# Kernel optimization log

Hardware: AMD Instinct MI355X
Metric: run time of the kernel (lower is better)

The kernel has to match this reference:

```python
import jax, jax.numpy as jnp
import numpy as np

N_NODES, N_EDGES, BATCH = 50000, 100000, 256
H = 64            # dim_hidden_features
D_NODE, D_EDGE, D_RBF = 110, 8, 8
D_SET = 2 * H     # Set2Set input_dim = 128, output_dim = 256
D_HID = 512
D_CAT = 54
MP_STEPS, S2S_ITERS = 4, 3


def setup_inputs() -> dict:
    key = jax.random.key(0)
    ks = iter(jax.random.split(key, 48))

    def nrm(shape, s=0.05):
        return jax.random.normal(next(ks), shape, dtype=jnp.float32) * s

    inp = {}
    inp["node_attribute"] = jax.random.normal(next(ks), (N_NODES, D_NODE), dtype=jnp.float32)
    inp["edge_attribute"] = jax.random.normal(next(ks), (N_EDGES, D_EDGE), dtype=jnp.float32)
    inp["edge_length"] = jax.random.uniform(next(ks), (N_EDGES,), dtype=jnp.float32)
    inp["src"] = jax.random.randint(next(ks), (N_EDGES,), 0, N_NODES, dtype=jnp.int32)
    inp["dst"] = jax.random.randint(next(ks), (N_EDGES,), 0, N_NODES, dtype=jnp.int32)
    inp["node_graph"] = jnp.sort(jax.random.randint(next(ks), (N_NODES,), 0, BATCH, dtype=jnp.int32))
    # atom_feature_projector
    inp["proj_W"] = nrm((D_NODE, H)); inp["proj_b"] = jnp.zeros((H,), jnp.float32)
    # RBF layer: centers ~ U(0,1), beta = 10 (per reset_parameters)
    inp["centers"] = jax.random.uniform(next(ks), (D_RBF,), dtype=jnp.float32)
    inp["beta"] = jnp.full((D_RBF,), 10.0, jnp.float32)
    # NNConv edge function: Linear(16 -> 64*64), plus NNConv bias
    inp["bond_W"] = nrm((D_EDGE + D_RBF, H * H)); inp["bond_b"] = jnp.zeros((H * H,), jnp.float32)
    inp["conv_b"] = jnp.zeros((H,), jnp.float32)
    # GRU (input H, hidden H); PyTorch layout (3H, in)
    inp["gru_Wih"] = nrm((3 * H, H)); inp["gru_Whh"] = nrm((3 * H, H))
    inp["gru_bih"] = jnp.zeros((3 * H,), jnp.float32); inp["gru_bhh"] = jnp.zeros((3 * H,), jnp.float32)
    # Set2Set LSTM: input 2*D_SET=256, hidden D_SET=128, 2 layers; PyTorch layout (4H, in)
    inp["lstm_Wih0"] = nrm((4 * D_SET, 2 * D_SET)); inp["lstm_Whh0"] = nrm((4 * D_SET, D_SET))
    inp["lstm_bih0"] = jnp.zeros((4 * D_SET,), jnp.float32); inp["lstm_bhh0"] = jnp.zeros((4 * D_SET,), jnp.float32)
    inp["lstm_Wih1"] = nrm((4 * D_SET, D_SET)); inp["lstm_Whh1"] = nrm((4 * D_SET, D_SET))
    inp["lstm_bih1"] = jnp.zeros((4 * D_SET,), jnp.float32); inp["lstm_bhh1"] = jnp.zeros((4 * D_SET,), jnp.float32)
    # sparsify: Linear(256 -> 512) + PReLU(init 0.25)
    inp["sp_W"] = nrm((2 * D_SET, D_HID)); inp["sp_b"] = jnp.zeros((D_HID,), jnp.float32)
    inp["prelu_a"] = jnp.array([0.25], jnp.float32)
    # catalyst1 head: hiddens[0] (512->512 ReLU, 512->512 Tanh) then outputs[0] (512->54)
    inp["h0_W1"] = nrm((D_HID, D_HID)); inp["h0_b1"] = jnp.zeros((D_HID,), jnp.float32)
    inp["h0_W2"] = nrm((D_HID, D_HID)); inp["h0_b2"] = jnp.zeros((D_HID,), jnp.float32)
    inp["out_W"] = nrm((D_HID, D_CAT)); inp["out_b"] = jnp.zeros((D_CAT,), jnp.float32)
    return inp


def _lstm_cell(x, h, c, Wih, Whh, bih, bhh):
    # PyTorch LSTM gate order: i, f, g, o
    g = x @ Wih.T + bih + h @ Whh.T + bhh
    i, f, gg, o = jnp.split(g, 4, axis=-1)
    c = jax.nn.sigmoid(f) * c + jax.nn.sigmoid(i) * jnp.tanh(gg)
    h = jax.nn.sigmoid(o) * jnp.tanh(c)
    return h, c


def reference(node_attribute, edge_attribute, edge_length, src, dst, node_graph,
              proj_W, proj_b, centers, beta, bond_W, bond_b, conv_b,
              gru_Wih, gru_Whh, gru_bih, gru_bhh,
              lstm_Wih0, lstm_Whh0, lstm_bih0, lstm_bhh0,
              lstm_Wih1, lstm_Whh1, lstm_bih1, lstm_bhh1,
              sp_W, sp_b, prelu_a, h0_W1, h0_b1, h0_W2, h0_b2, out_W, out_b):
    n_nodes = node_attribute.shape[0]
    # atom feature projection
    x = jax.nn.relu(node_attribute @ proj_W + proj_b)                       # (N, H)
    # edge features = [edge_attribute, RBF(length)]
    rbf = jnp.exp(-beta * (edge_length[:, None] - centers[None, :]) ** 2)   # (E, 8)
    efeat = jnp.concatenate([edge_attribute, rbf], axis=-1)                 # (E, 16)
    # NNConv per-edge weight matrix; edge features are constant over MP steps
    W_e = (efeat @ bond_W + bond_b).reshape(-1, H, H)                       # (E, H, H)

    feat, h = x, x
    for _ in range(MP_STEPS):
        # NNConv: message = h_src @ W_e, sum-aggregated at dst, plus bias
        m = jnp.einsum('ei,eio->eo', feat[src], W_e)                        # (E, H)
        agg = jax.ops.segment_sum(m, dst, num_segments=n_nodes) + conv_b    # (N, H)
        gx = jax.nn.relu(agg)
        # GRU cell (PyTorch gate order r, z, n)
        gi = gx @ gru_Wih.T + gru_bih
        gh = h @ gru_Whh.T + gru_bhh
        i_r, i_z, i_n = jnp.split(gi, 3, axis=-1)
        h_r, h_z, h_n = jnp.split(gh, 3, axis=-1)
        r = jax.nn.sigmoid(i_r + h_r)
        z = jax.nn.sigmoid(i_z + h_z)
        n = jnp.tanh(i_n + r * h_n)
        h = (1.0 - z) * n + z * h
        feat = h
    node_agg = jnp.concatenate([feat, x], axis=-1)                          # (N, 2H)

    # Set2Set pooling over graphs (segment softmax attention, 2-layer LSTM)
    B = BATCH
    h0 = c0 = jnp.zeros((B, D_SET), node_agg.dtype)
    h1 = c1 = jnp.zeros((B, D_SET), node_agg.dtype)
    q_star = jnp.zeros((B, 2 * D_SET), node_agg.dtype)
    for _ in range(S2S_ITERS):
        h0, c0 = _lstm_cell(q_star, h0, c0, lstm_Wih0, lstm_Whh0, lstm_bih0, lstm_bhh0)
        h1, c1 = _lstm_cell(h0, h1, c1, lstm_Wih1, lstm_Whh1, lstm_bih1, lstm_bhh1)
        q = h1                                                              # (B, 128)
        e = jnp.sum(node_agg * q[node_graph], axis=-1)                      # (N,)
        emax = jax.ops.segment_max(e, node_graph, num_segments=B)
        p = jnp.exp(e - emax[node_graph])
        denom = jax.ops.segment_sum(p, node_graph, num_segments=B)
        alpha = p / denom[node_graph]                                       # per-graph softmax
        r_out = jax.ops.segment_sum(node_agg * alpha[:, None], node_graph, num_segments=B)
        q_star = jnp.concatenate([q, r_out], axis=-1)                       # (B, 256)

    # sparsify (Linear + PReLU)
    feats = q_star @ sp_W + sp_b                                            # (B, 512)
    feats = jnp.where(feats >= 0, feats, prelu_a * feats)
    # catalyst1 head
    hid = jnp.tanh(jax.nn.relu(feats @ h0_W1 + h0_b1) @ h0_W2 + h0_b2)
    return jax.nn.softmax(hid @ out_W + out_b, axis=-1)                     # (B, 54)
```

## Files before the change

kernel.cpp:

```cpp
#include <hip/hip_runtime.h>
#include <math.h>

constexpr int N = 50000;
constexpr int E = 100000;
constexpr int B = 256;
constexpr int H = 64;
constexpr int DN = 110;
constexpr int NBLK = (E + 63) / 64;

#define DEV __device__ __forceinline__

typedef __attribute__((ext_vector_type(8))) short short8;
typedef __attribute__((ext_vector_type(4))) float floatx4;

DEV float sigf(float x) { return 1.0f / (1.0f + expf(-x)); }

DEV short f2bf(float f) {
    unsigned u = __float_as_uint(f);
    unsigned r = (u + 0x7fffu + ((u >> 16) & 1u)) >> 16;
    return (short)r;
}
DEV float bf2f(short s) { return __uint_as_float(((unsigned)(unsigned short)s) << 16); }

DEV void cvt8(const float* p, short8& hi, short8& lo) {
// ... 26 lines not shown
    int t = idx >> 6;
    int ntile = t % NT16;
    int kt = t / NT16;
    int quad = lane >> 4, col = lane & 15;
    int o = ntile * 16 + col;
    short hi[8], lo[8];
#pragma unroll
    for (int j = 0; j < 8; ++j) {
        int k = kt * 32 + quad * 8 + j;
        float v = 0.0f;
        if (o < ocap && k < kcap) v = trans ? W[(size_t)o * ld + k] : W[(size_t)k * ld + o];
        short hb = f2bf(v);
        hi[j] = hb;
        lo[j] = f2bf(v - bf2f(hb));
    }
    short* dh = out + (((size_t)(t * 2 + 0) * 64 + lane) * 8);
    short* dl = out + (((size_t)(t * 2 + 1) * 64 + lane) * 8);
#pragma unroll
    for (int j = 0; j < 8; ++j) { dh[j] = hi[j]; dl[j] = lo[j]; }
}

DEV void d_prepW(const float* __restrict__ bond_W, const float* __restrict__ bond_b,
                 short* __restrict__ wf, int idx) {
    int lane = idx & 63;
    int t = idx >> 6;
    int ks = t & 1;
    int nt = (t >> 1) & 3;
    int kk = t >> 3;
    const float* S = (kk < 16) ? (bond_W + kk * 4096) : bond_b;
    int quad = lane >> 4, col = lane & 15;
    short hi[8], lo[8];
#pragma unroll
    for (int j = 0; j < 8; ++j) {
        int i = ks * 32 + quad * 8 + j;
        float v = S[i * 64 + nt * 16 + col];
        short hb = f2bf(v);
        hi[j] = hb;
        lo[j] = f2bf(v - bf2f(hb));
    }
    short* dh = wf + (((size_t)(t * 2 + 0) * 64 + lane) * 8);
    short* dl = wf + (((size_t)(t * 2 + 1) * 64 + lane) * 8);
#pragma unroll
    for (int j = 0; j < 8; ++j) { dh[j] = hi[j]; dl[j] = lo[j]; }
}

__launch_bounds__(256)
__global__ void k_prep0(const float* lWih0, const float* lWhh0, const float* lWih1, const float* lWhh1,
                        float* lW0P, float* lU0P, float* lW1P, float* lU1P,
                        const float* bond_W, const float* bond_b, short* wf,
                        const float* gru_Wih, const float* gru_Whh, short* fgI, short* fgH,
                        const float* proj_W, short* fproj,
                        const float* ea, const float* el, const float* centers,
                        const float* beta, const int* epos, float* ef_t,
                        const int* ng, int* gs, int* ge,
                        float* zreg) {
    int idx = blockIdx.x * 256 + threadIdx.x;
    if (idx < 65536) { d_packpair(lWih0, lW0P, 256, idx); return; }
    idx -= 65536;
    if (idx < 32768) { d_packpair(lWhh0, lU0P, 128, idx); return; }
    idx -= 32768;
    if (idx < 32768) { d_packpair(lWih1, lW1P, 128, idx); return; }
    idx -= 32768;
    if (idx < 32768) { d_packpair(lWhh1, lU1P, 128, idx); return; }
    idx -= 32768;
    if (idx < 8704) { d_prepW(bond_W, bond_b, wf, idx); return; }
    idx -= 8704;
    if (idx < 1536) { d_prepB(gru_Wih, fgI, 12, 64, 1, 192, 64, idx); return; }
    idx -= 1536;
    if (idx < 1536) { d_prepB(gru_Whh, fgH, 12, 64, 1, 192, 64, idx); return; }
    idx -= 1536;
    if (idx < 1024) { d_prepB(proj_W, fproj, 4, 64, 0, 64, DN, idx); return; }
    idx -= 1024;
    if (idx < E) {
        int e = idx;
        int pos = epos[e];
        float L = el[e];
#pragma unroll
        for (int j = 0; j < 8; ++j) ef_t[(size_t)j * E + pos] = ea[e * 8 + j];
#pragma unroll
        for (int j = 0; j < 8; ++j) {
            float d = L - centers[j];
            ef_t[(size_t)(8 + j) * E + pos] = expf(-beta[j] * d * d);
        }
        ef_t[(size_t)16 * E + pos] = 1.0f;
        return;
    }
    idx -= E;
    if (idx < N) {
        int n = idx;
        int g = ng[n];
        int gp = (n == 0) ? -1 : ng[n - 1];
        if (g != gp) {
            gs[g] = n;
            if (n > 0) ge[gp] = n;
            for (int q = gp + 1; q < g; ++q) { gs[q] = 0; ge[q] = 0; }
        }
        if (n == N - 1) {
            ge[g] = N;
            for (int q = g + 1; q < B; ++q) { gs[q] = 0; ge[q] = 0; }
        }
        return;
    }
    idx -= N;
    if (idx < 196608) { zreg[idx] = 0.0f; return; }
}
constexpr int PREP0_TOTAL = 65536 + 3 * 32768 + 8704 + 2 * 1536 + 1024 + E + N + 196608;

__launch_bounds__(256)
__global__ void k_prephead(const float* sp_W, short* fsp, const float* h0_W1, short* fw1,
                           const float* h0_W2, short* fw2, const float* out_W, short* fow) {
    int idx = blockIdx.x * 256 + threadIdx.x;
    if (idx < 16384) { d_prepB(sp_W, fsp, 32, 512, 0, 512, 256, idx); return; }
    idx -= 16384;
    if (idx < 32768) { d_prepB(h0_W1, fw1, 32, 512, 0, 512, 512, idx); return; }
    idx -= 32768;
    if (idx < 32768) { d_prepB(h0_W2, fw2, 32, 512, 0, 512, 512, idx); return; }
    idx -= 32768;
    if (idx < 4096) { d_prepB(out_W, fow, 4, 54, 0, 54, 512, idx); return; }
}
constexpr int PREPH_TOTAL = 16384 + 2 * 32768 + 4096;

__global__ void k_deg(const int* __restrict__ dst, int* __restrict__ deg) {
    int e = blockIdx.x * 256 + threadIdx.x;
    if (e < E) atomicAdd(&deg[dst[e]], 1);
}
__global__ void k_scan1(const int* __restrict__ deg, int* __restrict__ bsum) {
    __shared__ int s[256];
    int b = blockIdx.x, tid = threadIdx.x;
    int idx = b * 256 + tid;
    s[tid] = (idx < N) ? deg[idx] : 0;
    __syncthreads();
    for (int st = 128; st > 0; st >>= 1) {
        if (tid < st) s[tid] += s[tid + st];
        __syncthreads();
    }
    if (tid == 0) bsum[b] = s[0];
}
__global__ void k_scan2p(int* __restrict__ bsum, int nb) {
    __shared__ int s[256];
    int tid = threadIdx.x;
    int v = (tid < nb) ? bsum[tid] : 0;
    s[tid] = v;
    __syncthreads();
    for (int off = 1; off < 256; off <<= 1) {
        int t = (tid >= off) ? s[tid - off] : 0;
        __syncthreads();
        s[tid] += t;
        __syncthreads();
    }
    if (tid < nb) bsum[tid] = s[tid] - v;
}
__global__ void k_scan3(const int* __restrict__ deg, const int* __restrict__ bsum,
                        int* __restrict__ cursor, int* __restrict__ roff) {
    __shared__ int s[256];
    int b = blockIdx.x, tid = threadIdx.x;
    int idx = b * 256 + tid;
    int v = (idx < N) ? deg[idx] : 0;
    s[tid] = v;
    __syncthreads();
    for (int off = 1; off < 256; off <<= 1) {
        int t = (tid >= off) ? s[tid - off] : 0;
        __syncthreads();
        s[tid] += t;
        __syncthreads();
    }
    if (idx < N) {
        int start = bsum[b] + s[tid] - v;
        cursor[idx] = start;
        roff[idx] = start;
    }
    if (idx == 0) roff[N] = E;
}
__global__ void k_scat(const int* __restrict__ src, const int* __restrict__ dst,
// ... 13 lines not shown
                        const float* __restrict__ b, float* __restrict__ x,
                        short* __restrict__ hs) {
    __shared__ float as[16 * 132];
    int tid = threadIdx.x, lane = tid & 63, nt = tid >> 6;
    int quad = lane >> 4, col = lane & 15;
    int s0 = blockIdx.x * 16;
    for (int i = tid; i < 16 * DN; i += 256) {
        int r = i / DN, c = i % DN;
        as[r * 132 + c] = na[(size_t)s0 * DN + i];
    }
    for (int i = tid; i < 16 * 22; i += 256) {
        int r = i / 22, c = DN + i % 22;
        as[r * 132 + c] = 0.0f;
    }
    __syncthreads();
    const short8* F = (const short8*)fp;
    floatx4 T = {0.0f, 0.0f, 0.0f, 0.0f};
#pragma unroll
    for (int kt = 0; kt < 4; ++kt) {
        const float* ap = as + col * 132 + kt * 32 + quad * 8;
        short8 ah, al;
#pragma unroll
        for (int j = 0; j < 8; ++j) {
            float v = ap[j];
            short hb = f2bf(v);
            ah[j] = hb;
            al[j] = f2bf(v - bf2f(hb));
        }
        int t = kt * 4 + nt;
        short8 bh = F[(t * 2 + 0) * 64 + lane];
        short8 bl = F[(t * 2 + 1) * 64 + lane];
        T = __builtin_amdgcn_mfma_f32_16x16x32_bf16(ah, bh, T, 0, 0, 0);
        T = __builtin_amdgcn_mfma_f32_16x16x32_bf16(al, bh, T, 0, 0, 0);
        T = __builtin_amdgcn_mfma_f32_16x16x32_bf16(ah, bl, T, 0, 0, 0);
    }
    int o = nt * 16 + col;
    float bo = b[o];
#pragma unroll
    for (int r = 0; r < 4; ++r) {
        int n = s0 + quad * 4 + r;
        float v = fmaxf(T[r] + bo, 0.0f);
        x[(size_t)n * 64 + o] = v;
        short hb = f2bf(v);
        hs[(size_t)n * 128 + o] = hb;
        hs[(size_t)n * 128 + 64 + o] = f2bf(v - bf2f(hb));
    }
}

__launch_bounds__(256)
__global__ void k_msgagg(const short* __restrict__ hs, const float* __restrict__ ef_t,
                         const short* __restrict__ wf, const int* __restrict__ srcp,
                         const int* __restrict__ dstp,
                         float* __restrict__ agg, float* __restrict__ bpart) {
    __shared__ int dsh[64];
    __shared__ int shprev;
    __shared__ float Csh[64][68];

    int tid = threadIdx.x;
    int e0 = blockIdx.x * 64;
    int lane = tid & 63;
    int nt = tid >> 6;
    int quad = lane >> 4, col = lane & 15;

    if (tid < 64) {
        int eg = e0 + tid;
        dsh[tid] = (eg < E) ? dstp[eg] : N;
    }
    if (tid == 0) shprev = (e0 == 0) ? -1 : dstp[e0 - 1];

    short8 Ah[4][2], Al[4][2];
#pragma unroll
    for (int mt = 0; mt < 4; ++mt) {
        int eg = e0 + mt * 16 + col;
        int s = (eg < E) ? srcp[eg] : 0;
        const short* hp = hs + (size_t)s * 128 + quad * 8;
#pragma unroll
        for (int ks = 0; ks < 2; ++ks) {
            Ah[mt][ks] = *(const short8*)(hp + ks * 32);
            Al[mt][ks] = *(const short8*)(hp + 64 + ks * 32);
        }
    }

    const short8* Wf = (const short8*)wf;
    const float* efb = ef_t + e0 + quad * 4;
    float C[4][4] = {};

#define LOADB(d0, d1, d2, d3, KK)                      \
    {                                                  \
        int tb_ = ((KK) * 4 + nt) * 2;                 \
        d0 = Wf[((tb_ + 0) * 2 + 0) * 64 + lane];      \
        d1 = Wf[((tb_ + 1) * 2 + 0) * 64 + lane];      \
        d2 = Wf[((tb_ + 0) * 2 + 1) * 64 + lane];      \
        d3 = Wf[((tb_ + 1) * 2 + 1) * 64 + lane];      \
    }

    short8 c0, c1, c2, c3, n0_, n1_, n2_, n3_, q0, q1, q2, q3;
    LOADB(c0, c1, c2, c3, 0);
    LOADB(n0_, n1_, n2_, n3_, 1);
    LOADB(q0, q1, q2, q3, 2);

#pragma unroll 1
    for (int kk = 0; kk < 17; ++kk) {
        int kn = kk + 3;
        if (kn > 16) kn = 16;
        short8 p0, p1, p2, p3;
        LOADB(p0, p1, p2, p3, kn);

        float4 ef0 = *(const float4*)(efb + (size_t)kk * E + 0);
        float4 ef1 = *(const float4*)(efb + (size_t)kk * E + 16);
        float4 ef2 = *(const float4*)(efb + (size_t)kk * E + 32);
        float4 ef3 = *(const float4*)(efb + (size_t)kk * E + 48);
        float4 efv[4] = {ef0, ef1, ef2, ef3};

#pragma unroll
        for (int mt = 0; mt < 4; ++mt) {
            floatx4 T = {0.0f, 0.0f, 0.0f, 0.0f};
            T = __builtin_amdgcn_mfma_f32_16x16x32_bf16(Ah[mt][0], c0, T, 0, 0, 0);
            T = __builtin_amdgcn_mfma_f32_16x16x32_bf16(Ah[mt][1], c1, T, 0, 0, 0);
            T = __builtin_amdgcn_mfma_f32_16x16x32_bf16(Al[mt][0], c0, T, 0, 0, 0);
            T = __builtin_amdgcn_mfma_f32_16x16x32_bf16(Al[mt][1], c1, T, 0, 0, 0);
            T = __builtin_amdgcn_mfma_f32_16x16x32_bf16(Ah[mt][0], c2, T, 0, 0, 0);
            T = __builtin_amdgcn_mfma_f32_16x16x32_bf16(Ah[mt][1], c3, T, 0, 0, 0);
            C[mt][0] += efv[mt].x * T[0];
            C[mt][1] += efv[mt].y * T[1];
            C[mt][2] += efv[mt].z * T[2];
            C[mt][3] += efv[mt].w * T[3];
        }
        c0 = n0_; c1 = n1_; c2 = n2_; c3 = n3_;
        n0_ = q0; n1_ = q1; n2_ = q2; n3_ = q3;
        q0 = p0; q1 = p1; q2 = p2; q3 = p3;
    }
#undef LOADB

#pragma unroll
    for (int mt = 0; mt < 4; ++mt)
#pragma unroll
        for (int r = 0; r < 4; ++r)
            Csh[mt * 16 + quad * 4 + r][nt * 16 + col] = C[mt][r];
    __syncthreads();

    if (tid < 64) {
        int c = tid;
        int prevd = shprev;
        int firstd = dsh[0];
        for (int q = prevd + 1; q < firstd; ++q) agg[(size_t)q * 64 + c] = 0.0f;
        int cur = firstd;
        float acc = 0.0f;
        bool owned = (e0 == 0) || (firstd != prevd);
        bool done = false;
        for (int r = 0; r < 64; ++r) {
            int d = dsh[r];
            if (d != cur) {
                if (owned) agg[(size_t)cur * 64 + c] = acc;
                else bpart[(size_t)blockIdx.x * 64 + c] = acc;
                int dc = (d < N) ? d : N;
                for (int q = cur + 1; q < dc; ++q) agg[(size_t)q * 64 + c] = 0.0f;
                cur = d;
                acc = 0.0f;
                owned = true;
                if (cur >= N) { done = true; break; }
            }
            acc += Csh[r][c];
        }
        if (!done) {
            if (owned) agg[(size_t)cur * 64 + c] = acc;
            else bpart[(size_t)blockIdx.x * 64 + c] = acc;
        }
    }
}

__launch_bounds__(256)
__global__ void k_gru4(const float* agg, const float* __restrict__ bpart,
                       const int* __restrict__ roff, const float* __restrict__ conv_b,
                       short* __restrict__ hs,
                       const short* __restrict__ fI, const short* __restrict__ fH,
                       const float* __restrict__ bih, const float* __restrict__ bhh,
                       float* hf) {
    __shared__ float aggS[32 * 65];
    __shared__ short hsS[32 * 132];
// ... 100 lines not shown
                aH[mt][g] = __builtin_amdgcn_mfma_f32_16x16x32_bf16(Hh[mt][ks], bHl[g], aH[mt][g], 0, 0, 0);
            }
        }
    }

    int o = nt * 16 + col;
    float br = bih[o], bz = bih[64 + o], bn = bih[128 + o];
    float cr = bhh[o], cz = bhh[64 + o], cn = bhh[128 + o];
#pragma unroll
    for (int mt = 0; mt < 2; ++mt) {
#pragma unroll
        for (int r = 0; r < 4; ++r) {
            int row = mt * 16 + quad * 4 + r;
            float rg = sigf(aI[mt][0][r] + br + aH[mt][0][r] + cr);
            float z  = sigf(aI[mt][1][r] + bz + aH[mt][1][r] + cz);
            float ng = tanhf(aI[mt][2][r] + bn + rg * (aH[mt][2][r] + cn));
            float hold = bf2f(hsS[row * 132 + o]) + bf2f(hsS[row * 132 + 64 + o]);
            aggS[row * 65 + o] = (1.0f - z) * ng + z * hold;
        }
    }
    __syncthreads();

#pragma unroll
    for (int it = 0; it < 2; ++it) {
        int i = tid * 8 + it * 2048;
        int r = i >> 7, c = i & 127;
        int node = n0 + r;
        if (node < N) {
            bool hiP = (c < 64);
            int f0 = hiP ? c : (c - 64);
            short8 v;
#pragma unroll
            for (int j = 0; j < 8; ++j) {
                float hv = aggS[r * 65 + f0 + j];
                short hb = f2bf(hv);
                v[j] = hiP ? hb : f2bf(hv - bf2f(hb));
            }
            *(short8*)(hs + (size_t)node * 128 + c) = v;
        }
    }
    if (hf) {
#pragma unroll
        for (int it = 0; it < 2; ++it) {
            int i = tid * 4 + it * 1024;
            int r = i >> 6, c = i & 63;
            int node = n0 + r;
            if (node < N)
                *(float4*)(hf + (size_t)node * 64 + c) = *(const float4*)&aggS[r * 65 + c];
        }
    }
}

__launch_bounds__(256)
__global__ void k_s2s(float* __restrict__ h0, float* __restrict__ c0,
                      float* __restrict__ h1, float* __restrict__ c1,
                      float* __restrict__ q_star,
                      const float* __restrict__ W0P, const float* __restrict__ U0P,
                      const float* __restrict__ b0i, const float* __restrict__ b0h,
                      const float* __restrict__ W1P, const float* __restrict__ U1P,
                      const float* __restrict__ b1i, const float* __restrict__ b1h,
                      const float* __restrict__ hf, const float* __restrict__ x,
                      const int* __restrict__ gs, const int* __restrict__ ge) {
    __shared__ float xb[256], hb[128], gb[512], h0n[128], qv[128];
    __shared__ float mrg[4][2][64];
    __shared__ float ml[4][2];
    int g = blockIdx.x, tid = threadIdx.x;
    xb[tid] = q_star[g * 256 + tid];
    if (tid < 128) hb[tid] = h0[g * 128 + tid];
    __syncthreads();
    float g0 = b0i[tid] + b0h[tid];
    float g1 = b0i[tid + 256] + b0h[tid + 256];
    for (int i = 0; i < 256; ++i) {
        float xx = xb[i];
        float2 w = *(const float2*)(W0P + 2 * (i * 256 + tid));
        g0 += xx * w.x;
        g1 += xx * w.y;
    }
    for (int i = 0; i < 128; ++i) {
        float hh = hb[i];
        float2 w = *(const float2*)(U0P + 2 * (i * 256 + tid));
        g0 += hh * w.x;
        g1 += hh * w.y;
    }
    gb[tid] = g0; gb[tid + 256] = g1;
    __syncthreads();
    if (tid < 128) {
        float ii = gb[tid], ff = gb[128 + tid], gg = gb[256 + tid], oo = gb[384 + tid];
        float c = sigf(ff) * c0[g * 128 + tid] + sigf(ii) * tanhf(gg);
        float hn = sigf(oo) * tanhf(c);
        c0[g * 128 + tid] = c; h0[g * 128 + tid] = hn; h0n[tid] = hn;
        hb[tid] = h1[g * 128 + tid];
    }
    __syncthreads();
    float ga = b1i[tid] + b1h[tid];
    float gbv = b1i[tid + 256] + b1h[tid + 256];
    for (int i = 0; i < 128; ++i) {
        float xx = h0n[i], hh = hb[i];
        float2 w1 = *(const float2*)(W1P + 2 * (i * 256 + tid));
        float2 u1 = *(const float2*)(U1P + 2 * (i * 256 + tid));
        ga  += xx * w1.x + hh * u1.x;
        gbv += xx * w1.y + hh * u1.y;
    }
    gb[tid] = ga; gb[tid + 256] = gbv;
    __syncthreads();
    if (tid < 128) {
        float ii = gb[tid], ff = gb[128 + tid], gg = gb[256 + tid], oo = gb[384 + tid];
        float c = sigf(ff) * c1[g * 128 + tid] + sigf(ii) * tanhf(gg);
        float hn = sigf(oo) * tanhf(c);
        c1[g * 128 + tid] = c; h1[g * 128 + tid] = hn;
        q_star[g * 256 + tid] = hn;
        qv[tid] = hn;
    }
    __syncthreads();
    int s0v = gs[g], s1v = ge[g];
    int lane = tid & 63, grp = tid >> 6;
    float qh = qv[lane], qx = qv[64 + lane];
    float mM = -INFINITY, lL = 0.0f, nh = 0.0f, nx = 0.0f;
    for (int n = s0v + grp; n < s1v; n += 16) {
        float hv[4], xv[4], e[4];
#pragma unroll
        for (int j = 0; j < 4; ++j) {
            int nj = n + 4 * j;
            int nc = (nj < s1v) ? nj : n;
            hv[j] = hf[(size_t)nc * 64 + lane];
            xv[j] = x[(size_t)nc * 64 + lane];
            e[j] = hv[j] * qh + xv[j] * qx;
        }
#pragma unroll
        for (int off = 32; off; off >>= 1) {
#pragma unroll
            for (int j = 0; j < 4; ++j) e[j] += __shfl_xor(e[j], off, 64);
        }
#pragma unroll
        for (int j = 0; j < 4; ++j)
            if (n + 4 * j >= s1v) e[j] = -INFINITY;
        float mb = fmaxf(fmaxf(e[0], e[1]), fmaxf(e[2], e[3]));
        float mn = fmaxf(mM, mb);
        float sc = expf(mM - mn);
        float w0 = expf(e[0] - mn), w1 = expf(e[1] - mn);
        float w2 = expf(e[2] - mn), w3 = expf(e[3] - mn);
        lL = lL * sc + ((w0 + w1) + (w2 + w3));
        nh = nh * sc + ((w0 * hv[0] + w1 * hv[1]) + (w2 * hv[2] + w3 * hv[3]));
        nx = nx * sc + ((w0 * xv[0] + w1 * xv[1]) + (w2 * xv[2] + w3 * xv[3]));
        mM = mn;
    }
    mrg[grp][0][lane] = nh;
    mrg[grp][1][lane] = nx;
    if (lane == 0) { ml[grp][0] = mM; ml[grp][1] = lL; }
    __syncthreads();
    if (tid < 128) {
        int half = tid >> 6, dl = tid & 63;
        float M = -INFINITY;
#pragma unroll
        for (int i = 0; i < 4; ++i) M = fmaxf(M, ml[i][0]);
        float L = 0.0f, NUM = 0.0f;
#pragma unroll
        for (int i = 0; i < 4; ++i) {
            float sc = expf(ml[i][0] - M);
            L += ml[i][1] * sc;
            NUM += mrg[i][half][dl] * sc;
        }
        q_star[g * 256 + 128 + tid] = (s1v > s0v) ? NUM / L : 0.0f;
    }
}

template<int MODE>
__launch_bounds__(256)
__global__ void k_hgemm(const float* __restrict__ A, const short* __restrict__ Bf,
                        const float* __restrict__ bias, const float* __restrict__ pa,
                        float* __restrict__ Cout, int K, int NT16) {
    int tid = threadIdx.x, lane = tid & 63, nt = tid >> 6;
    int quad = lane >> 4, col = lane & 15;
    int s0 = blockIdx.x * 16;
    int ntile = blockIdx.y * 4 + nt;
    int NoutTot = NT16 * 16;
    const short8* F = (const short8*)Bf;
    floatx4 T = {0.0f, 0.0f, 0.0f, 0.0f};
    const float* ap = A + (size_t)(s0 + col) * K + quad * 8;
    int KT = K >> 5;
#pragma unroll 4
    for (int kt = 0; kt < KT; ++kt) {
        short8 ah, al;
        cvt8(ap + kt * 32, ah, al);
        int t = kt * NT16 + ntile;
        short8 bh = F[(t * 2 + 0) * 64 + lane];
        short8 bl = F[(t * 2 + 1) * 64 + lane];
        T = __builtin_amdgcn_mfma_f32_16x16x32_bf16(ah, bh, T, 0, 0, 0);
        T = __builtin_amdgcn_mfma_f32_16x16x32_bf16(al, bh, T, 0, 0, 0);
        T = __builtin_amdgcn_mfma_f32_16x16x32_bf16(ah, bl, T, 0, 0, 0);
    }
    int o = ntile * 16 + col;
    float b = bias[o];
    float a = (MODE == 0) ? pa[0] : 0.0f;
#pragma unroll
    for (int r = 0; r < 4; ++r) {
        float v = T[r] + b;
        if (MODE == 0) v = (v >= 0.0f) ? v : a * v;
        if (MODE == 1) v = fmaxf(v, 0.0f);
        if (MODE == 2) v = tanhf(v);
        Cout[(size_t)(s0 + quad * 4 + r) * NoutTot + o] = v;
    }
}

__launch_bounds__(256)
__global__ void k_hout(const float* __restrict__ A, const short* __restrict__ Bf,
                       const float* __restrict__ ob, float* __restrict__ out) {
    __shared__ float sm[16][64];
    __shared__ float smax[16], sinv[16];
    int tid = threadIdx.x, lane = tid & 63, nt = tid >> 6;
    int quad = lane >> 4, col = lane & 15;
    int s0 = blockIdx.x * 16;
    const short8* F = (const short8*)Bf;
    floatx4 T = {0.0f, 0.0f, 0.0f, 0.0f};
    const float* ap = A + (size_t)(s0 + col) * 512 + quad * 8;
#pragma unroll 4
    for (int kt = 0; kt < 16; ++kt) {
        short8 ah, al;
        cvt8(ap + kt * 32, ah, al);
        int t = kt * 4 + nt;
        short8 bh = F[(t * 2 + 0) * 64 + lane];
        short8 bl = F[(t * 2 + 1) * 64 + lane];
        T = __builtin_amdgcn_mfma_f32_16x16x32_bf16(ah, bh, T, 0, 0, 0);
        T = __builtin_amdgcn_mfma_f32_16x16x32_bf16(al, bh, T, 0, 0, 0);
        T = __builtin_amdgcn_mfma_f32_16x16x32_bf16(ah, bl, T, 0, 0, 0);
    }
    int o = nt * 16 + col;
    float b = (o < 54) ? ob[o] : 0.0f;
#pragma unroll
    for (int r = 0; r < 4; ++r)
        sm[quad * 4 + r][o] = (o < 54) ? (T[r] + b) : -1e30f;
    __syncthreads();
    if (tid < 16) {
        float m = -INFINITY;
        for (int j = 0; j < 54; ++j) m = fmaxf(m, sm[tid][j]);
        float s = 0.0f;
        for (int j = 0; j < 54; ++j) s += expf(sm[tid][j] - m);
        smax[tid] = m;
        sinv[tid] = 1.0f / s;
    }
    __syncthreads();
    for (int idx = tid; idx < 16 * 54; idx += 256) {
        int srow = idx / 54, oo = idx % 54;
        out[(size_t)(s0 + srow) * 54 + oo] = expf(sm[srow][oo] - smax[srow]) * sinv[srow];
    }
}

extern "C" void kernel_launch(void* const* d_in, const int* in_sizes, int n_in,
                              void* d_out, int out_size, void* d_ws, size_t ws_size,
                              hipStream_t stream) {
    const float* node_attr = (const float*)d_in[0];
    const float* edge_attr = (const float*)d_in[1];
    const float* edge_len  = (const float*)d_in[2];
    const int*   src       = (const int*)d_in[3];
    const int*   dst       = (const int*)d_in[4];
    const int*   node_grph = (const int*)d_in[5];
    const float* proj_W    = (const float*)d_in[6];
    const float* proj_b    = (const float*)d_in[7];
    const float* centers   = (const float*)d_in[8];
    const float* beta      = (const float*)d_in[9];
    const float* bond_W    = (const float*)d_in[10];
    const float* bond_b    = (const float*)d_in[11];
    const float* conv_b    = (const float*)d_in[12];
    const float* gru_Wih   = (const float*)d_in[13];
    const float* gru_Whh   = (const float*)d_in[14];
    const float* gru_bih   = (const float*)d_in[15];
    const float* gru_bhh   = (const float*)d_in[16];
    const float* lWih0     = (const float*)d_in[17];
    const float* lWhh0     = (const float*)d_in[18];
    const float* lbih0     = (const float*)d_in[19];
    const float* lbhh0     = (const float*)d_in[20];
    const float* lWih1     = (const float*)d_in[21];
    const float* lWhh1     = (const float*)d_in[22];
    const float* lbih1     = (const float*)d_in[23];
    const float* lbhh1     = (const float*)d_in[24];
    const float* sp_W      = (const float*)d_in[25];
    const float* sp_b      = (const float*)d_in[26];
    const float* prelu_a   = (const float*)d_in[27];
    const float* h0_W1     = (const float*)d_in[28];
    const float* h0_b1     = (const float*)d_in[29];
    const float* h0_W2     = (const float*)d_in[30];
    const float* h0_b2     = (const float*)d_in[31];
    const float* out_W     = (const float*)d_in[32];
    const float* out_b     = (const float*)d_in[33];
    float* out = (float*)d_out;

    float* ws = (float*)d_ws;
    size_t off = 0;
    float* x      = ws + off; off += (size_t)N * 64;
    float* hsf    = ws + off; off += (size_t)N * 64;
    float* ef_t   = ws + off; off += (size_t)E * 17;
    float* agg    = ws + off; off += (size_t)N * 64;
    float* wfrag  = ws + off; off += 17 * 16 * 64 * 8 / 2;
    float* fgI    = ws + off; off += 2 * 64 * 192 / 2;
    float* fgH    = ws + off; off += 2 * 64 * 192 / 2;
    float* fproj  = ws + off; off += 16 * 1024 / 2;
    float* lW0P   = ws + off; off += 256 * 512;
    float* lU0P   = ws + off; off += 128 * 512;
    float* lW1P   = ws + off; off += 128 * 512;
    float* lU1P   = ws + off; off += 128 * 512;
    float* h0     = ws + off; off += B * 128;
    float* c0     = ws + off; off += B * 128;
    float* h1     = ws + off; off += B * 128;
    float* c1     = ws + off; off += B * 128;
    float* q_star = ws + off; off += B * 256;
    float* bpart  = ws + off; off += (size_t)NBLK * 64;
    int* gs       = (int*)(ws + off); off += B;
    int* ge       = (int*)(ws + off); off += B;
    int* deg      = (int*)(ws + off); off += N;
    int* cursor   = (int*)(ws + off); off += N;
    int* roff     = (int*)(ws + off); off += N + 1;
    int* bsum     = (int*)(ws + off); off += 256;
    int* srcp     = (int*)(ws + off); off += E;
    int* epos     = (int*)(ws + off); off += E;
    int* dstp     = (int*)(ws + off); off += E;

    short* hs = (short*)hsf;

    short* fsp = (short*)ef_t;
    short* fw1 = (short*)(ef_t + 131072);
    short* fw2 = (short*)(ef_t + 131072 + 262144);
    short* fow = (short*)(ef_t + 131072 + 2 * 262144);
    float* hb1 = ef_t + 131072 + 2 * 262144 + 32768;
    float* hb2 = hb1 + 131072;

    constexpr int NB = (N + 255) / 256;

    k_izero<<<NB, 256, 0, stream>>>(deg, N);
    k_deg<<<(E + 255) / 256, 256, 0, stream>>>(dst, deg);
    k_scan1<<<NB, 256, 0, stream>>>(deg, bsum);
    k_scan2p<<<1, 256, 0, stream>>>(bsum, NB);
    k_scan3<<<NB, 256, 0, stream>>>(deg, bsum, cursor, roff);
    k_scat<<<(E + 255) / 256, 256, 0, stream>>>(src, dst, cursor, srcp, epos, dstp);

    k_prep0<<<(PREP0_TOTAL + 255) / 256, 256, 0, stream>>>(
        lWih0, lWhh0, lWih1, lWhh1, lW0P, lU0P, lW1P, lU1P,
        bond_W, bond_b, (short*)wfrag, gru_Wih, gru_Whh, (short*)fgI, (short*)fgH,
        proj_W, (short*)fproj,
        edge_attr, edge_len, centers, beta, epos, ef_t,
        node_grph, gs, ge, h0);

    k_projm<<<N / 16, 256, 0, stream>>>(node_attr, (const short*)fproj, proj_b, x, hs);

    for (int step = 0; step < 4; ++step) {
        k_msgagg<<<NBLK, 256, 0, stream>>>(hs, ef_t, (const short*)wfrag, srcp, dstp,
                                           agg, bpart);
        k_gru4<<<(N + 31) / 32, 256, 0, stream>>>(agg, bpart, roff, conv_b, hs,
                                                  (const short*)fgI, (const short*)fgH,
                                                  gru_bih, gru_bhh,
                                                  (step == 3) ? agg : nullptr);
    }

    k_prephead<<<(PREPH_TOTAL + 255) / 256, 256, 0, stream>>>(
        sp_W, fsp, h0_W1, fw1, h0_W2, fw2, out_W, fow);

    for (int it = 0; it < 3; ++it) {
        k_s2s<<<B, 256, 0, stream>>>(h0, c0, h1, c1, q_star,
                                     lW0P, lU0P, lbih0, lbhh0,
                                     lW1P, lU1P, lbih1, lbhh1,
                                     agg, x, gs, ge);
    }

    k_hgemm<0><<<dim3(16, 8), 256, 0, stream>>>(q_star, fsp, sp_b, prelu_a, hb1, 256, 32);
    k_hgemm<1><<<dim3(16, 8), 256, 0, stream>>>(hb1, fw1, h0_b1, nullptr, hb2, 512, 32);
    k_hgemm<2><<<dim3(16, 8), 256, 0, stream>>>(hb2, fw2, h0_b2, nullptr, hb1, 512, 32);
    k_hout<<<16, 256, 0, stream>>>(hb1, fow, out_b, out);
}
```

Before: 696.6 us.

## Fuse Set2Set iterations and head GEMMs into single kernels, stage edge features in LDS

The three Set2Set launches are merged into one kernel that keeps the LSTM state in shared memory and skips the matmuls against zero state on the first iteration. The head weight prep is folded into the tail of that kernel. The four head GEMM launches become one kernel that keeps its activations in LDS. In the message kernel, edge features and source indices are staged into shared memory before the MFMA loop instead of being loaded from global memory inside it. The aim is to cut launch count, global round-trips of intermediates and the zeroing pass, at the cost of more LDS use and an extra barrier in the message kernel.

```diff
diff --git a/kernel.cpp b/kernel.cpp
--- a/kernel.cpp
+++ b/kernel.cpp
@@ -102,8 +102,7 @@
                         const float* proj_W, short* fproj,
                         const float* ea, const float* el, const float* centers,
                         const float* beta, const int* epos, float* ef_t,
-                        const int* ng, int* gs, int* ge,
-                        float* zreg) {
+                        const int* ng, int* gs, int* ge) {
     int idx = blockIdx.x * 256 + threadIdx.x;
     if (idx < 65536) { d_packpair(lWih0, lW0P, 256, idx); return; }
     idx -= 65536;
@@ -151,24 +150,8 @@
         }
         return;
     }
-    idx -= N;
-    if (idx < 196608) { zreg[idx] = 0.0f; return; }
-}
-constexpr int PREP0_TOTAL = 65536 + 3 * 32768 + 8704 + 2 * 1536 + 1024 + E + N + 196608;
-
-__launch_bounds__(256)
-__global__ void k_prephead(const float* sp_W, short* fsp, const float* h0_W1, short* fw1,
-                           const float* h0_W2, short* fw2, const float* out_W, short* fow) {
-    int idx = blockIdx.x * 256 + threadIdx.x;
-    if (idx < 16384) { d_prepB(sp_W, fsp, 32, 512, 0, 512, 256, idx); return; }
-    idx -= 16384;
-    if (idx < 32768) { d_prepB(h0_W1, fw1, 32, 512, 0, 512, 512, idx); return; }
-    idx -= 32768;
-    if (idx < 32768) { d_prepB(h0_W2, fw2, 32, 512, 0, 512, 512, idx); return; }
-    idx -= 32768;
-    if (idx < 4096) { d_prepB(out_W, fow, 4, 54, 0, 54, 512, idx); return; }
-}
-constexpr int PREPH_TOTAL = 16384 + 2 * 32768 + 4096;
+}
+constexpr int PREP0_TOTAL = 65536 + 3 * 32768 + 8704 + 2 * 1536 + 1024 + E + N;
 
 __global__ void k_deg(const int* __restrict__ dst, int* __restrict__ deg) {
     int e = blockIdx.x * 256 + threadIdx.x;
@@ -288,6 +271,8 @@
                          const short* __restrict__ wf, const int* __restrict__ srcp,
                          const int* __restrict__ dstp,
                          float* __restrict__ agg, float* __restrict__ bpart) {
+    __shared__ float efs[17 * 64];
+    __shared__ int srcs[64];
     __shared__ int dsh[64];
     __shared__ int shprev;
     __shared__ float Csh[64][68];
@@ -300,15 +285,21 @@
 
     if (tid < 64) {
         int eg = e0 + tid;
+        srcs[tid] = (eg < E) ? srcp[eg] : 0;
         dsh[tid] = (eg < E) ? dstp[eg] : N;
     }
     if (tid == 0) shprev = (e0 == 0) ? -1 : dstp[e0 - 1];
+    for (int i = tid; i < 17 * 64; i += 256) {
+        int kk = i >> 6, e = i & 63;
+        int eg = e0 + e;
+        efs[i] = (eg < E) ? ef_t[(size_t)kk * E + eg] : 0.0f;
+    }
+    __syncthreads();
 
     short8 Ah[4][2], Al[4][2];
 #pragma unroll
     for (int mt = 0; mt < 4; ++mt) {
-        int eg = e0 + mt * 16 + col;
-        int s = (eg < E) ? srcp[eg] : 0;
+        int s = srcs[mt * 16 + col];
         const short* hp = hs + (size_t)s * 128 + quad * 8;
 #pragma unroll
         for (int ks = 0; ks < 2; ++ks) {
@@ -318,7 +309,6 @@
     }
 
     const short8* Wf = (const short8*)wf;
-    const float* efb = ef_t + e0 + quad * 4;
     float C[4][4] = {};
 
 #define LOADB(d0, d1, d2, d3, KK)                      \
@@ -341,12 +331,6 @@
         if (kn > 16) kn = 16;
         short8 p0, p1, p2, p3;
         LOADB(p0, p1, p2, p3, kn);
-
-        float4 ef0 = *(const float4*)(efb + (size_t)kk * E + 0);
-        float4 ef1 = *(const float4*)(efb + (size_t)kk * E + 16);
-        float4 ef2 = *(const float4*)(efb + (size_t)kk * E + 32);
-        float4 ef3 = *(const float4*)(efb + (size_t)kk * E + 48);
-        float4 efv[4] = {ef0, ef1, ef2, ef3};
 
 #pragma unroll
         for (int mt = 0; mt < 4; ++mt) {
@@ -357,10 +341,11 @@
             T = __builtin_amdgcn_mfma_f32_16x16x32_bf16(Al[mt][1], c1, T, 0, 0, 0);
             T = __builtin_amdgcn_mfma_f32_16x16x32_bf16(Ah[mt][0], c2, T, 0, 0, 0);
             T = __builtin_amdgcn_mfma_f32_16x16x32_bf16(Ah[mt][1], c3, T, 0, 0, 0);
-            C[mt][0] += efv[mt].x * T[0];
-            C[mt][1] += efv[mt].y * T[1];
-            C[mt][2] += efv[mt].z * T[2];
-            C[mt][3] += efv[mt].w * T[3];
+            float4 ef = *(const float4*)&efs[kk * 64 + mt * 16 + quad * 4];
+            C[mt][0] += ef.x * T[0];
+            C[mt][1] += ef.y * T[1];
+            C[mt][2] += ef.z * T[2];
+            C[mt][3] += ef.w * T[3];
         }
         c0 = n0_; c1 = n1_; c2 = n2_; c3 = n3_;
         n0_ = q0; n1_ = q1; n2_ = q2; n3_ = q3;
@@ -567,183 +552,265 @@
 }
 
 __launch_bounds__(256)
-__global__ void k_s2s(float* __restrict__ h0, float* __restrict__ c0,
-                      float* __restrict__ h1, float* __restrict__ c1,
-                      float* __restrict__ q_star,
-                      const float* __restrict__ W0P, const float* __restrict__ U0P,
-                      const float* __restrict__ b0i, const float* __restrict__ b0h,
-                      const float* __restrict__ W1P, const float* __restrict__ U1P,
-                      const float* __restrict__ b1i, const float* __restrict__ b1h,
-                      const float* __restrict__ hf, const float* __restrict__ x,
-                      const int* __restrict__ gs, const int* __restrict__ ge) {
-    __shared__ float xb[256], hb[128], gb[512], h0n[128], qv[128];
+__global__ void k_s2s3(float* __restrict__ q_star,
+                       const float* __restrict__ W0P, const float* __restrict__ U0P,
+                       const float* __restrict__ b0i, const float* __restrict__ b0h,
+                       const float* __restrict__ W1P, const float* __restrict__ U1P,
+                       const float* __restrict__ b1i, const float* __restrict__ b1h,
+                       const float* __restrict__ hf, const float* __restrict__ x,
+                       const int* __restrict__ gs, const int* __restrict__ ge,
+                       const float* sp_W, short* fsp, const float* h0_W1, short* fw1,
+                       const float* h0_W2, short* fw2, const float* out_W, short* fow) {
+    __shared__ float xb[256], h0b[128], c0b[128], h1b[128], c1b[128];
+    __shared__ float gb[512], h0n[128], qv[128];
     __shared__ float mrg[4][2][64];
     __shared__ float ml[4][2];
     int g = blockIdx.x, tid = threadIdx.x;
-    xb[tid] = q_star[g * 256 + tid];
-    if (tid < 128) hb[tid] = h0[g * 128 + tid];
-    __syncthreads();
-    float g0 = b0i[tid] + b0h[tid];
-    float g1 = b0i[tid + 256] + b0h[tid + 256];
-    for (int i = 0; i < 256; ++i) {
-        float xx = xb[i];
-        float2 w = *(const float2*)(W0P + 2 * (i * 256 + tid));
-        g0 += xx * w.x;
-        g1 += xx * w.y;
-    }
-    for (int i = 0; i < 128; ++i) {
-        float hh = hb[i];
-        float2 w = *(const float2*)(U0P + 2 * (i * 256 + tid));
-        g0 += hh * w.x;
-        g1 += hh * w.y;
-    }
-    gb[tid] = g0; gb[tid + 256] = g1;
-    __syncthreads();
-    if (tid < 128) {
-        float ii = gb[tid], ff = gb[128 + tid], gg = gb[256 + tid], oo = gb[384 + tid];
-        float c = sigf(ff) * c0[g * 128 + tid] + sigf(ii) * tanhf(gg);
-        float hn = sigf(oo) * tanhf(c);
-        c0[g * 128 + tid] = c; h0[g * 128 + tid] = hn; h0n[tid] = hn;
-        hb[tid] = h1[g * 128 + tid];
-    }
-    __syncthreads();
-    float ga = b1i[tid] + b1h[tid];
-    float gbv = b1i[tid + 256] + b1h[tid + 256];
-    for (int i = 0; i < 128; ++i) {
-        float xx = h0n[i], hh = hb[i];
-        float2 w1 = *(const float2*)(W1P + 2 * (i * 256 + tid));
-        float2 u1 = *(const float2*)(U1P + 2 * (i * 256 + tid));
-        ga  += xx * w1.x + hh * u1.x;
-        gbv += xx * w1.y + hh * u1.y;
-    }
-    gb[tid] = ga; gb[tid + 256] = gbv;
-    __syncthreads();
-    if (tid < 128) {
-        float ii = gb[tid], ff = gb[128 + tid], gg = gb[256 + tid], oo = gb[384 + tid];
-        float c = sigf(ff) * c1[g * 128 + tid] + sigf(ii) * tanhf(gg);
-        float hn = sigf(oo) * tanhf(c);
-        c1[g * 128 + tid] = c; h1[g * 128 + tid] = hn;
-        q_star[g * 256 + tid] = hn;
-        qv[tid] = hn;
-    }
-    __syncthreads();
+    int lane = tid & 63, grp = tid >> 6;
     int s0v = gs[g], s1v = ge[g];
-    int lane = tid & 63, grp = tid >> 6;
-    float qh = qv[lane], qx = qv[64 + lane];
-    float mM = -INFINITY, lL = 0.0f, nh = 0.0f, nx = 0.0f;
-    for (int n = s0v + grp; n < s1v; n += 16) {
-        float hv[4], xv[4], e[4];
-#pragma unroll
-        for (int j = 0; j < 4; ++j) {
-            int nj = n + 4 * j;
-            int nc = (nj < s1v) ? nj : n;
-            hv[j] = hf[(size_t)nc * 64 + lane];
-            xv[j] = x[(size_t)nc * 64 + lane];
-            e[j] = hv[j] * qh + xv[j] * qx;
-        }
-#pragma unroll
-        for (int off = 32; off; off >>= 1) {
-#pragma unroll
-            for (int j = 0; j < 4; ++j) e[j] += __shfl_xor(e[j], off, 64);
-        }
-#pragma unroll
-        for (int j = 0; j < 4; ++j)
-            if (n + 4 * j >= s1v) e[j] = -INFINITY;
-        float mb = fmaxf(fmaxf(e[0], e[1]), fmaxf(e[2], e[3]));
-        float mn = fmaxf(mM, mb);
-        float sc = expf(mM - mn);
-        float w0 = expf(e[0] - mn), w1 = expf(e[1] - mn);
-        float w2 = expf(e[2] - mn), w3 = expf(e[3] - mn);
-        lL = lL * sc + ((w0 + w1) + (w2 + w3));
-        nh = nh * sc + ((w0 * hv[0] + w1 * hv[1]) + (w2 * hv[2] + w3 * hv[3]));
-        nx = nx * sc + ((w0 * xv[0] + w1 * xv[1]) + (w2 * xv[2] + w3 * xv[3]));
-        mM = mn;
-    }
-    mrg[grp][0][lane] = nh;
-    mrg[grp][1][lane] = nx;
-    if (lane == 0) { ml[grp][0] = mM; ml[grp][1] = lL; }
-    __syncthreads();
-    if (tid < 128) {
-        int half = tid >> 6, dl = tid & 63;
-        float M = -INFINITY;
-#pragma unroll
-        for (int i = 0; i < 4; ++i) M = fmaxf(M, ml[i][0]);
-        float L = 0.0f, NUM = 0.0f;
-#pragma unroll
-        for (int i = 0; i < 4; ++i) {
-            float sc = expf(ml[i][0] - M);
-            L += ml[i][1] * sc;
-            NUM += mrg[i][half][dl] * sc;
-        }
-        q_star[g * 256 + 128 + tid] = (s1v > s0v) ? NUM / L : 0.0f;
-    }
-}
-
-template<int MODE>
+    xb[tid] = 0.0f;
+    if (tid < 128) { h0b[tid] = 0.0f; c0b[tid] = 0.0f; h1b[tid] = 0.0f; c1b[tid] = 0.0f; }
+    __syncthreads();
+
+    for (int it = 0; it < 3; ++it) {
+        float g0 = b0i[tid] + b0h[tid];
+        float g1 = b0i[tid + 256] + b0h[tid + 256];
+        if (it > 0) {
+            for (int i = 0; i < 256; ++i) {
+                float xx = xb[i];
+                float2 w = *(const float2*)(W0P + 2 * (i * 256 + tid));
+                g0 += xx * w.x;
+                g1 += xx * w.y;
+            }
+            for (int i = 0; i < 128; ++i) {
+                float hh = h0b[i];
+                float2 w = *(const float2*)(U0P + 2 * (i * 256 + tid));
+                g0 += hh * w.x;
+                g1 += hh * w.y;
+            }
+        }
+        gb[tid] = g0; gb[tid + 256] = g1;
+        __syncthreads();
+        if (tid < 128) {
+            float ii = gb[tid], ff = gb[128 + tid], gg = gb[256 + tid], oo = gb[384 + tid];
+            float c = sigf(ff) * c0b[tid] + sigf(ii) * tanhf(gg);
+            float hn = sigf(oo) * tanhf(c);
+            c0b[tid] = c; h0b[tid] = hn; h0n[tid] = hn;
+        }
+        __syncthreads();
+        float ga = b1i[tid] + b1h[tid];
+        float gbv = b1i[tid + 256] + b1h[tid + 256];
+        for (int i = 0; i < 128; ++i) {
+            float xx = h0n[i];
+            float2 w1 = *(const float2*)(W1P + 2 * (i * 256 + tid));
+            ga += xx * w1.x;
+            gbv += xx * w1.y;
+        }
+        if (it > 0) {
+            for (int i = 0; i < 128; ++i) {
+                float hh = h1b[i];
+                float2 u1 = *(const float2*)(U1P + 2 * (i * 256 + tid));
+                ga += hh * u1.x;
+                gbv += hh * u1.y;
+            }
+        }
+        gb[tid] = ga; gb[tid + 256] = gbv;
+        __syncthreads();
+        if (tid < 128) {
+            float ii = gb[tid], ff = gb[128 + tid], gg = gb[256 + tid], oo = gb[384 + tid];
+            float c = sigf(ff) * c1b[tid] + sigf(ii) * tanhf(gg);
+            float hn = sigf(oo) * tanhf(c);
+            c1b[tid] = c; h1b[tid] = hn; qv[tid] = hn;
+        }
+        __syncthreads();
+        float qh = qv[lane], qx = qv[64 + lane];
+        float mM = -INFINITY, lL = 0.0f, nh = 0.0f, nx = 0.0f;
+        for (int n = s0v + grp; n < s1v; n += 16) {
+            float hv[4], xv[4], e[4];
+#pragma unroll
+            for (int j = 0; j < 4; ++j) {
+                int nj = n + 4 * j;
+                int nc = (nj < s1v) ? nj : n;
+                hv[j] = hf[(size_t)nc * 64 + lane];
+                xv[j] = x[(size_t)nc * 64 + lane];
+                e[j] = hv[j] * qh + xv[j] * qx;
+            }
+#pragma unroll
+            for (int off = 32; off; off >>= 1) {
+#pragma unroll
+                for (int j = 0; j < 4; ++j) e[j] += __shfl_xor(e[j], off, 64);
+            }
+#pragma unroll
+            for (int j = 0; j < 4; ++j)
+                if (n + 4 * j >= s1v) e[j] = -INFINITY;
+            float mb = fmaxf(fmaxf(e[0], e[1]), fmaxf(e[2], e[3]));
+            float mn = fmaxf(mM, mb);
+            float sc = expf(mM - mn);
+            float w0 = expf(e[0] - mn), w1 = expf(e[1] - mn);
+            float w2 = expf(e[2] - mn), w3 = expf(e[3] - mn);
+            lL = lL * sc + ((w0 + w1) + (w2 + w3));
+            nh = nh * sc + ((w0 * hv[0] + w1 * hv[1]) + (w2 * hv[2] + w3 * hv[3]));
+            nx = nx * sc + ((w0 * xv[0] + w1 * xv[1]) + (w2 * xv[2] + w3 * xv[3]));
+            mM = mn;
+        }
+        mrg[grp][0][lane] = nh;
+        mrg[grp][1][lane] = nx;
+        if (lane == 0) { ml[grp][0] = mM; ml[grp][1] = lL; }
+        __syncthreads();
+        if (tid < 128) {
+            int half = tid >> 6, dl = tid & 63;
+            float M = -INFINITY;
+#pragma unroll
+            for (int i = 0; i < 4; ++i) M = fmaxf(M, ml[i][0]);
+            float L = 0.0f, NUM = 0.0f;
+#pragma unroll
+            for (int i = 0; i < 4; ++i) {
+                float sc = expf(ml[i][0] - M);
+                L += ml[i][1] * sc;
+                NUM += mrg[i][half][dl] * sc;
+            }
+            xb[128 + tid] = (s1v > s0v) ? NUM / L : 0.0f;
+            xb[tid] = qv[tid];
+        }
+        __syncthreads();
+    }
+    q_star[g * 256 + tid] = xb[tid];
+
+    for (int ii2 = tid; ii2 < 336; ii2 += 256) {
+        int idx = g * 336 + ii2;
+        if (idx < 16384) { d_prepB(sp_W, fsp, 32, 512, 0, 512, 256, idx); continue; }
+        idx -= 16384;
+        if (idx < 32768) { d_prepB(h0_W1, fw1, 32, 512, 0, 512, 512, idx); continue; }
+        idx -= 32768;
+        if (idx < 32768) { d_prepB(h0_W2, fw2, 32, 512, 0, 512, 512, idx); continue; }
+        idx -= 32768;
+        d_prepB(out_W, fow, 4, 54, 0, 54, 512, idx);
+    }
+}
+
 __launch_bounds__(256)
-__global__ void k_hgemm(const float* __restrict__ A, const short* __restrict__ Bf,
-                        const float* __restrict__ bias, const float* __restrict__ pa,
-                        float* __restrict__ Cout, int K, int NT16) {
-    int tid = threadIdx.x, lane = tid & 63, nt = tid >> 6;
-    int quad = lane >> 4, col = lane & 15;
-    int s0 = blockIdx.x * 16;
-    int ntile = blockIdx.y * 4 + nt;
-    int NoutTot = NT16 * 16;
-    const short8* F = (const short8*)Bf;
-    floatx4 T = {0.0f, 0.0f, 0.0f, 0.0f};
-    const float* ap = A + (size_t)(s0 + col) * K + quad * 8;
-    int KT = K >> 5;
-#pragma unroll 4
-    for (int kt = 0; kt < KT; ++kt) {
-        short8 ah, al;
-        cvt8(ap + kt * 32, ah, al);
-        int t = kt * NT16 + ntile;
-        short8 bh = F[(t * 2 + 0) * 64 + lane];
-        short8 bl = F[(t * 2 + 1) * 64 + lane];
-        T = __builtin_amdgcn_mfma_f32_16x16x32_bf16(ah, bh, T, 0, 0, 0);
-        T = __builtin_amdgcn_mfma_f32_16x16x32_bf16(al, bh, T, 0, 0, 0);
-        T = __builtin_amdgcn_mfma_f32_16x16x32_bf16(ah, bl, T, 0, 0, 0);
-    }
-    int o = ntile * 16 + col;
-    float b = bias[o];
-    float a = (MODE == 0) ? pa[0] : 0.0f;
-#pragma unroll
-    for (int r = 0; r < 4; ++r) {
-        float v = T[r] + b;
-        if (MODE == 0) v = (v >= 0.0f) ? v : a * v;
-        if (MODE == 1) v = fmaxf(v, 0.0f);
-        if (MODE == 2) v = tanhf(v);
-        Cout[(size_t)(s0 + quad * 4 + r) * NoutTot + o] = v;
-    }
-}
-
-__launch_bounds__(256)
-__global__ void k_hout(const float* __restrict__ A, const short* __restrict__ Bf,
-                       const float* __restrict__ ob, float* __restrict__ out) {
+__global__ void k_head(const float* __restrict__ q_star,
+                       const short* __restrict__ fsp, const float* __restrict__ sp_b,
+                       const float* __restrict__ pa,
+                       const short* __restrict__ fw1, const float* __restrict__ hb1,
+                       const short* __restrict__ fw2, const float* __restrict__ hb2,
+                       const short* __restrict__ fow, const float* __restrict__ ob,
+                       float* __restrict__ out) {
+    __shared__ float A0[16 * 260];
+    __shared__ float A1[16 * 516];
+    __shared__ float A2[16 * 516];
     __shared__ float sm[16][64];
     __shared__ float smax[16], sinv[16];
     int tid = threadIdx.x, lane = tid & 63, nt = tid >> 6;
     int quad = lane >> 4, col = lane & 15;
     int s0 = blockIdx.x * 16;
-    const short8* F = (const short8*)Bf;
-    floatx4 T = {0.0f, 0.0f, 0.0f, 0.0f};
-    const float* ap = A + (size_t)(s0 + col) * 512 + quad * 8;
+
+    for (int i = tid * 4; i < 4096; i += 1024) {
+        float4 v = *(const float4*)(q_star + (size_t)s0 * 256 + i);
+        int r = i >> 8, c = i & 255;
+        *(float4*)&A0[r * 260 + c] = v;
+    }
+    __syncthreads();
+    float aP = pa[0];
+
+    {
+        const short8* F = (const short8*)fsp;
+#pragma unroll 1
+        for (int t8 = 0; t8 < 8; ++t8) {
+            int ntile = t8 * 4 + nt;
+            floatx4 T = {0.0f, 0.0f, 0.0f, 0.0f};
+#pragma unroll
+            for (int kt = 0; kt < 8; ++kt) {
+                short8 ah, al;
+                cvt8(&A0[col * 260 + kt * 32 + quad * 8], ah, al);
+                int t = kt * 32 + ntile;
+                short8 bh = F[(t * 2 + 0) * 64 + lane];
+                short8 bl = F[(t * 2 + 1) * 64 + lane];
+                T = __builtin_amdgcn_mfma_f32_16x16x32_bf16(ah, bh, T, 0, 0, 0);
+                T = __builtin_amdgcn_mfma_f32_16x16x32_bf16(al, bh, T, 0, 0, 0);
+                T = __builtin_amdgcn_mfma_f32_16x16x32_bf16(ah, bl, T, 0, 0, 0);
+            }
+            int o = ntile * 16 + col;
+            float b = sp_b[o];
+#pragma unroll
+            for (int r = 0; r < 4; ++r) {
+                float v = T[r] + b;
+                v = (v >= 0.0f) ? v : aP * v;
+                A1[(quad * 4 + r) * 516 + o] = v;
+            }
+        }
+    }
+    __syncthreads();
+    {
+        const short8* F = (const short8*)fw1;
+#pragma unroll 1
+        for (int t8 = 0; t8 < 8; ++t8) {
+            int ntile = t8 * 4 + nt;
+            floatx4 T = {0.0f, 0.0f, 0.0f, 0.0f};
 #pragma unroll 4
-    for (int kt = 0; kt < 16; ++kt) {
-        short8 ah, al;
-        cvt8(ap + kt * 32, ah, al);
-        int t = kt * 4 + nt;
-        short8 bh = F[(t * 2 + 0) * 64 + lane];
-        short8 bl = F[(t * 2 + 1) * 64 + lane];
-        T = __builtin_amdgcn_mfma_f32_16x16x32_bf16(ah, bh, T, 0, 0, 0);
-        T = __builtin_amdgcn_mfma_f32_16x16x32_bf16(al, bh, T, 0, 0, 0);
-        T = __builtin_amdgcn_mfma_f32_16x16x32_bf16(ah, bl, T, 0, 0, 0);
-    }
-    int o = nt * 16 + col;
-    float b = (o < 54) ? ob[o] : 0.0f;
-#pragma unroll
-    for (int r = 0; r < 4; ++r)
-        sm[quad * 4 + r][o] = (o < 54) ? (T[r] + b) : -1e30f;
+            for (int kt = 0; kt < 16; ++kt) {
+                short8 ah, al;
+                cvt8(&A1[col * 516 + kt * 32 + quad * 8], ah, al);
+                int t = kt * 32 + ntile;
+                short8 bh = F[(t * 2 + 0) * 64 + lane];
+                short8 bl = F[(t * 2 + 1) * 64 + lane];
+                T = __builtin_amdgcn_mfma_f32_16x16x32_bf16(ah, bh, T, 0, 0, 0);
+                T = __builtin_amdgcn_mfma_f32_16x16x32_bf16(al, bh, T, 0, 0, 0);
+                T = __builtin_amdgcn_mfma_f32_16x16x32_bf16(ah, bl, T, 0, 0, 0);
+            }
+            int o = ntile * 16 + col;
+            float b = hb1[o];
+#pragma unroll
+            for (int r = 0; r < 4; ++r)
+                A2[(quad * 4 + r) * 516 + o] = fmaxf(T[r] + b, 0.0f);
+        }
+    }
+    __syncthreads();
+    {
+        const short8* F = (const short8*)fw2;
+#pragma unroll 1
+        for (int t8 = 0; t8 < 8; ++t8) {
+            int ntile = t8 * 4 + nt;
+            floatx4 T = {0.0f, 0.0f, 0.0f, 0.0f};
+#pragma unroll 4
+            for (int kt = 0; kt < 16; ++kt) {
+                short8 ah, al;
+                cvt8(&A2[col * 516 + kt * 32 + quad * 8], ah, al);
+                int t = kt * 32 + ntile;
+                short8 bh = F[(t * 2 + 0) * 64 + lane];
+                short8 bl = F[(t * 2 + 1) * 64 + lane];
+                T = __builtin_amdgcn_mfma_f32_16x16x32_bf16(ah, bh, T, 0, 0, 0);
+                T = __builtin_amdgcn_mfma_f32_16x16x32_bf16(al, bh, T, 0, 0, 0);
+                T = __builtin_amdgcn_mfma_f32_16x16x32_bf16(ah, bl, T, 0, 0, 0);
+            }
+            int o = ntile * 16 + col;
+            float b = hb2[o];
+#pragma unroll
+            for (int r = 0; r < 4; ++r)
+                A1[(quad * 4 + r) * 516 + o] = tanhf(T[r] + b);
+        }
+    }
+    __syncthreads();
+    {
+        const short8* F = (const short8*)fow;
+        floatx4 T = {0.0f, 0.0f, 0.0f, 0.0f};
+#pragma unroll 4
+        for (int kt = 0; kt < 16; ++kt) {
+            short8 ah, al;
+            cvt8(&A1[col * 516 + kt * 32 + quad * 8], ah, al);
+            int t = kt * 4 + nt;
+            short8 bh = F[(t * 2 + 0) * 64 + lane];
+            short8 bl = F[(t * 2 + 1) * 64 + lane];
+            T = __builtin_amdgcn_mfma_f32_16x16x32_bf16(ah, bh, T, 0, 0, 0);
+            T = __builtin_amdgcn_mfma_f32_16x16x32_bf16(al, bh, T, 0, 0, 0);
+            T = __builtin_amdgcn_mfma_f32_16x16x32_bf16(ah, bl, T, 0, 0, 0);
+        }
+        int o = nt * 16 + col;
+        float b = (o < 54) ? ob[o] : 0.0f;
+#pragma unroll
+        for (int r = 0; r < 4; ++r)
+            sm[quad * 4 + r][o] = (o < 54) ? (T[r] + b) : -1e30f;
+    }
     __syncthreads();
     if (tid < 16) {
         float m = -INFINITY;
@@ -813,10 +880,6 @@
     float* lU0P   = ws + off; off += 128 * 512;
     float* lW1P   = ws + off; off += 128 * 512;
     float* lU1P   = ws + off; off += 128 * 512;
-    float* h0     = ws + off; off += B * 128;
-    float* c0     = ws + off; off += B * 128;
-    float* h1     = ws + off; off += B * 128;
-    float* c1     = ws + off; off += B * 128;
     float* q_star = ws + off; off += B * 256;
     float* bpart  = ws + off; off += (size_t)NBLK * 64;
     int* gs       = (int*)(ws + off); off += B;
@@ -835,8 +898,6 @@
     short* fw1 = (short*)(ef_t + 131072);
     short* fw2 = (short*)(ef_t + 131072 + 262144);
     short* fow = (short*)(ef_t + 131072 + 2 * 262144);
-    float* hb1 = ef_t + 131072 + 2 * 262144 + 32768;
-    float* hb2 = hb1 + 131072;
 
     constexpr int NB = (N + 255) / 256;
 
@@ -852,7 +913,7 @@
         bond_W, bond_b, (short*)wfrag, gru_Wih, gru_Whh, (short*)fgI, (short*)fgH,
         proj_W, (short*)fproj,
         edge_attr, edge_len, centers, beta, epos, ef_t,
-        node_grph, gs, ge, h0);
+        node_grph, gs, ge);
 
     k_projm<<<N / 16, 256, 0, stream>>>(node_attr, (const short*)fproj, proj_b, x, hs);
 
@@ -865,18 +926,12 @@
                                                   (step == 3) ? agg : nullptr);
     }
 
-    k_prephead<<<(PREPH_TOTAL + 255) / 256, 256, 0, stream>>>(
-        sp_W, fsp, h0_W1, fw1, h0_W2, fw2, out_W, fow);
-
-    for (int it = 0; it < 3; ++it) {
-        k_s2s<<<B, 256, 0, stream>>>(h0, c0, h1, c1, q_star,
-                                     lW0P, lU0P, lbih0, lbhh0,
-                                     lW1P, lU1P, lbih1, lbhh1,
-                                     agg, x, gs, ge);
-    }
-
-    k_hgemm<0><<<dim3(16, 8), 256, 0, stream>>>(q_star, fsp, sp_b, prelu_a, hb1, 256, 32);
-    k_hgemm<1><<<dim3(16, 8), 256, 0, stream>>>(hb1, fw1, h0_b1, nullptr, hb2, 512, 32);
-    k_hgemm<2><<<dim3(16, 8), 256, 0, stream>>>(hb2, fw2, h0_b2, nullptr, hb1, 512, 32);
-    k_hout<<<16, 256, 0, stream>>>(hb1, fow, out_b, out);
-}
+    k_s2s3<<<B, 256, 0, stream>>>(q_star,
+                                  lW0P, lU0P, lbih0, lbhh0,
+                                  lW1P, lU1P, lbih1, lbhh1,
+                                  agg, x, gs, ge,
+                                  sp_W, fsp, h0_W1, fw1, h0_W2, fw2, out_W, fow);
+
+    k_head<<<16, 256, 0, stream>>>(q_star, fsp, sp_b, prelu_a,
+                                   fw1, h0_b1, fw2, h0_b2, fow, out_b, out);
+}
```

Measured after the change: 710.0 us. Within noise of the previous version (+1.9%).
